# Optimization experiments

Hardware: AMD Instinct MI355X
Metric: run time of the kernel (lower is better)

## Reference

```python
import jax, jax.numpy as jnp
import numpy as np

C, NSET, K, GC = 64, 32, 3, 4
G = C // GC          # 16 KBA groups
EPS = 1e-6


def conv2d(x, w, b=None, groups=1, padding=0):
    out = jax.lax.conv_general_dilated(
        x, w, (1, 1), [(padding, padding), (padding, padding)],
        dimension_numbers=('NCHW', 'OIHW', 'NCHW'), feature_group_count=groups)
    if b is not None:
        out = out + b[None, :, None, None]
    return out


def layernorm2d(x, w, b):
    mu = jnp.mean(x, axis=1, keepdims=True)
    var = jnp.var(x, axis=1, keepdims=True)
    return (x - mu) / jnp.sqrt(var + EPS) * w[None, :, None, None] + b[None, :, None, None]


def simple_gate(x):
    a, b = jnp.split(x, 2, axis=1)
    return a * b


def kba(x, att, kb_b, kb_w):
    # x: [B,C,H,W], att: [B,nset,H,W], kb_b: [1,nset,C], kb_w: [1,nset,C*(C//G)*K*K]
    B, C_, H, W = x.shape
    KK = K * K
    cg = C_ // G  # channels per group
    att2 = att.reshape(B, NSET, H * W).transpose(0, 2, 1)            # [B,HW,nset]
    bias = att2 @ kb_b[0]                                             # [B,HW,C]
    attk = (att2 @ kb_w[0]).reshape(B, H * W, G, cg, cg * KK)         # per-pixel kernels
    pad = K // 2
    xp = jnp.pad(x, ((0, 0), (0, 0), (pad, pad), (pad, pad)))
    # torch.unfold ordering: feature index = c*KK + ki*K + kj
    patches = jnp.stack([xp[:, :, i:i + H, j:j + W]
                         for i in range(K) for j in range(K)], axis=2)  # [B,C,KK,H,W]
    uf = patches.reshape(B, G, cg * KK, H * W).transpose(0, 3, 1, 2)    # [B,HW,G,cg*KK]
    out = jnp.einsum('bpgod,bpgd->bpgo', attk, uf).reshape(B, H * W, C_) + bias
    return out.transpose(0, 2, 1).reshape(B, C_, H, W)


def fca(x, fc1_w, fc1_b, fc2_w, fc2_b, fsca_w, fsca_b):
    f = jnp.fft.fft2(x, norm='ortho')                      # over (H,W)
    cf = jnp.concatenate([f.real, f.imag], axis=1)         # [B,2C,H,W]
    t = conv2d(simple_gate(conv2d(cf, fc1_w, fc1_b)), fc2_w, fc2_b)
    r, im = jnp.split(t, 2, axis=1)
    ra = conv2d(jnp.mean(r, axis=(2, 3), keepdims=True), fsca_w, fsca_b)
    ia = conv2d(jnp.mean(im, axis=(2, 3), keepdims=True), fsca_w, fsca_b)
    fn = (r + r * ra) + 1j * (im + im * ia)
    return jnp.abs(jnp.fft.ifft2(fn, norm='ortho'))


def reference(inp, n1_w, n1_b, n2_w, n2_b, sca_w, sca_b, c11a_w, c11a_b, c11b_w, c11b_b,
              c1_w, c1_b, c21_w, c21_b, c2a_w, c2a_b, c2c_w, c2c_b, c211_w, c211_b,
              c3_w, c3_b, kb_w, kb_b, ga1, attgamma, beta, gamma,
              fc1_w, fc1_b, fc2_w, fc2_b, fsca_w, fsca_b):
    x = layernorm2d(inp, n1_w, n1_b)
    sca = conv2d(jnp.mean(x, axis=(2, 3), keepdims=True), sca_w, sca_b)
    x1 = conv2d(conv2d(x, c11a_w, c11a_b), c11b_w, c11b_b, groups=C // 4, padding=2)
    att = conv2d(simple_gate(conv2d(x, c2a_w, c2a_b, groups=32, padding=1)),
                 c2c_w, c2c_b) * attgamma + conv2d(x, c211_w, c211_b)
    uf = conv2d(conv2d(x, c1_w, c1_b), c21_w, c21_b, groups=C, padding=1)
    xk = kba(uf, att, kb_b, kb_w) * ga1 + uf
    x = xk * x1 * sca
    x = conv2d(x, c3_w, c3_b)
    y = inp + x * beta
    z = fca(layernorm2d(y, n2_w, n2_b), fc1_w, fc1_b, fc2_w, fc2_b, fsca_w, fsca_b)
    return y + z * gamma


def setup_inputs() -> dict:
    key = jax.random.key(0)
    B, H, W = 2, 160, 160
    ks = jax.random.split(key, 32)
    def rn(i, shape, s=0.05):
        return jax.random.normal(ks[i], shape, dtype=jnp.float32) * s
    return dict(
        inp=rn(0, (B, C, H, W), 1.0),
        n1_w=jnp.ones((C,), jnp.float32), n1_b=jnp.zeros((C,), jnp.float32),
        n2_w=jnp.ones((C,), jnp.float32), n2_b=jnp.zeros((C,), jnp.float32),
        sca_w=rn(1, (C, C, 1, 1)), sca_b=rn(2, (C,)),
        c11a_w=rn(3, (C, C, 1, 1)), c11a_b=rn(4, (C,)),
        c11b_w=rn(5, (C, 4, 5, 5)), c11b_b=rn(6, (C,)),
        c1_w=rn(7, (C, C, 1, 1)), c1_b=rn(8, (C,)),
        c21_w=rn(9, (C, 1, 3, 3)), c21_b=rn(10, (C,)),
        c2a_w=rn(11, (32, 2, 3, 3)), c2a_b=rn(12, (32,)),
        c2c_w=rn(13, (NSET, 16, 1, 1)), c2c_b=rn(14, (NSET,)),
        c211_w=rn(15, (NSET, C, 1, 1)), c211_b=rn(16, (NSET,)),
        c3_w=rn(17, (C, C, 1, 1)), c3_b=rn(18, (C,)),
        kb_w=rn(19, (1, NSET, C * (C // G) * K * K)),
        kb_b=rn(20, (1, NSET, C)),
        ga1=jnp.full((1, C, 1, 1), 0.01, jnp.float32),
        attgamma=jnp.full((1, NSET, 1, 1), 0.01, jnp.float32),
        beta=jnp.full((1, C, 1, 1), 0.01, jnp.float32),
        gamma=jnp.full((1, C, 1, 1), 0.01, jnp.float32),
        fc1_w=rn(21, (4 * C, 2 * C, 1, 1)), fc1_b=rn(22, (4 * C,)),
        fc2_w=rn(23, (2 * C, 2 * C, 1, 1)), fc2_b=rn(24, (2 * C,)),
        fsca_w=rn(25, (C, C, 1, 1)), fsca_b=rn(26, (C,)),
    )
```

## Files before the change

### kernel.cpp

```cpp
#include <hip/hip_runtime.h>
#include <hip/hip_bf16.h>

typedef __hip_bfloat16 bf16;
typedef __attribute__((ext_vector_type(8))) short short8;
typedef __attribute__((ext_vector_type(4))) float f32x4;
typedef __attribute__((ext_vector_type(4))) unsigned short u16x4;

#define Hh 160
#define Wd 160
#define HWp (Hh*Wd)
#define Bn 2
#define Cc 64
#define NPIX (Bn*HWp)
#define SCL 0.07905694150420949f
#define TWO_PI_160 0.039269908169872414f

static __device__ __forceinline__ float b2f(bf16 x) { return __bfloat162float(x); }
static __device__ __forceinline__ bf16 f2b(float f) { return __float2bfloat16(f); }
static __device__ __forceinline__ unsigned short f2bu(float f) {
  union { bf16 h; unsigned short u; } z; z.h = __float2bfloat16(f); return z.u;
}
static __device__ __forceinline__ float ubf(unsigned short u) {
  union { unsigned int i; float f; } z; z.i = ((unsigned int)u) << 16; return z.f;
}

__global__ void k_ln(const float* __restrict__ in, const float* __restrict__ w,
                     const float* __restrict__ bb, bf16* __restrict__ out) {
  __shared__ float2 sm[4][64];
  int t = threadIdx.x;
  int pxl = t & 63, cq = t >> 6;
  int pix = blockIdx.x * 64 + pxl;
  int b = pix / HWp, p = pix - b * HWp;
  const float* src = in + ((size_t)b * Cc + cq * 16) * HWp + p;
  float v[16];
  float s = 0.f, s2 = 0.f;
  #pragma unroll
  for (int i = 0; i < 16; i++) {
    v[i] = src[(size_t)i * HWp];
    s += v[i]; s2 += v[i] * v[i];
  }
  sm[cq][pxl] = make_float2(s, s2);
  __syncthreads();
  float S = 0.f, S2 = 0.f;
  #pragma unroll
  for (int k = 0; k < 4; k++) { float2 z = sm[k][pxl]; S += z.x; S2 += z.y; }
  float mu = S * (1.f / 64.f);
  float var = S2 * (1.f / 64.f) - mu * mu;
  float rs = rsqrtf(fmaxf(var, 0.f) + 1e-6f);
  bf16* dst = out + ((size_t)b * Cc + cq * 16) * HWp + p;
  #pragma unroll
  for (int i = 0; i < 16; i++) {
    int c = cq * 16 + i;
    dst[(size_t)i * HWp] = f2b((v[i] - mu) * rs * w[c] + bb[c]);
  }
}

__global__ void k_meanhw(const bf16* __restrict__ in, float* __restrict__ out) {
  int bc = blockIdx.x;
  const bf16* src = in + (size_t)bc * HWp;
  int t = threadIdx.x;
  float s = 0.f;
  for (int i = t; i < HWp; i += 256) s += b2f(src[i]);
  __shared__ float sm[256];
  sm[t] = s; __syncthreads();
  for (int off = 128; off; off >>= 1) { if (t < off) sm[t] += sm[t + off]; __syncthreads(); }
  if (t == 0) out[bc] = sm[0] * (1.f / HWp);
}

__global__ void k_meanhw2(const bf16* __restrict__ in0, const bf16* __restrict__ in1,
                          float* __restrict__ out) {
  int bc = blockIdx.x;
  const bf16* src = (bc < 128) ? (in0 + (size_t)bc * HWp) : (in1 + (size_t)(bc - 128) * HWp);
  int t = threadIdx.x;
  float s = 0.f;
  for (int i = t; i < HWp; i += 256) s += b2f(src[i]);
  __shared__ float sm[256];
  sm[t] = s; __syncthreads();
  for (int off = 128; off; off >>= 1) { if (t < off) sm[t] += sm[t + off]; __syncthreads(); }
  if (t == 0) out[bc] = sm[0] * (1.f / HWp);
}

__global__ void k_small_mv(const float* __restrict__ xin, const float* __restrict__ w,
                           const float* __restrict__ bias, float* __restrict__ out, int addone) {
  int t = threadIdx.x;
  int b = t >> 6, o = t & 63;
  float acc = bias[o];
  for (int k = 0; k < 64; k++) acc += w[o * 64 + k] * xin[b * 64 + k];
  out[t] = addone ? (1.f + acc) : acc;
}

__global__ void k_small_mv2(const float* __restrict__ xin, const float* __restrict__ w,
                            const float* __restrict__ bias, float* __restrict__ out) {
  int t = threadIdx.x;
  int half = t >> 7, r = t & 127;
  int b = r >> 6, o = r & 63;
  const float* x = xin + half * 128 + b * 64;
  float acc = bias[o];
  for (int k = 0; k < 64; k++) acc += w[o * 64 + k] * x[k];
  out[half * 128 + r] = 1.f + acc;
}

__global__ void k_c2a4(const bf16* __restrict__ in, const float* __restrict__ w,
                       const float* __restrict__ bias, bf16* __restrict__ out) {
  int t = threadIdx.x;
  int o = blockIdx.y, b = blockIdx.z;
  int pq = blockIdx.x * 256 + t;
  int h = pq / 40, x4 = (pq - h * 40) * 4;
  float bs = bias[o];
  float acc[4] = {bs, bs, bs, bs};
  #pragma unroll
  for (int ci = 0; ci < 2; ci++) {
    const unsigned short* src = (const unsigned short*)in + ((size_t)b * Cc + o * 2 + ci) * HWp;
    float wv[9];
    #pragma unroll
    for (int i = 0; i < 9; i++) wv[i] = w[(o * 2 + ci) * 9 + i];
    #pragma unroll
    for (int ki = 0; ki < 3; ki++) {
      int hh = h + ki - 1;
      if ((unsigned)hh >= Hh) continue;
      const unsigned short* row = src + hh * Wd + x4;
      float v[6];
      u16x4 m = *(const u16x4*)row;
      v[1] = ubf(m[0]); v[2] = ubf(m[1]); v[3] = ubf(m[2]); v[4] = ubf(m[3]);
      v[0] = (x4 > 0) ? ubf(row[-1]) : 0.f;
      v[5] = (x4 + 4 < Wd) ? ubf(row[4]) : 0.f;
      #pragma unroll
      for (int j = 0; j < 4; j++)
        #pragma unroll
        for (int kj = 0; kj < 3; kj++)
          acc[j] = fmaf(wv[ki * 3 + kj], v[j + kj], acc[j]);
    }
  }
  u16x4 pk;
  #pragma unroll
  for (int j = 0; j < 4; j++) pk[j] = f2bu(acc[j]);
  *(u16x4*)((unsigned short*)out + ((size_t)b * 32 + o) * HWp + h * Wd + x4) = pk;
}

__global__ void k_c21dw4(const bf16* __restrict__ in, const float* __restrict__ w,
                         const float* __restrict__ bias, bf16* __restrict__ out) {
  int t = threadIdx.x;
  int c = blockIdx.y, b = blockIdx.z;
  int pq = blockIdx.x * 256 + t;
  int h = pq / 40, x4 = (pq - h * 40) * 4;
  const unsigned short* src = (const unsigned short*)in + ((size_t)b * Cc + c) * HWp;
  float wv[9];
  #pragma unroll
  for (int i = 0; i < 9; i++) wv[i] = w[c * 9 + i];
  float bs = bias[c];
  float acc[4] = {bs, bs, bs, bs};
  #pragma unroll
  for (int ki = 0; ki < 3; ki++) {
    int hh = h + ki - 1;
    if ((unsigned)hh >= Hh) continue;
    const unsigned short* row = src + hh * Wd + x4;
    float v[6];
    u16x4 m = *(const u16x4*)row;
    v[1] = ubf(m[0]); v[2] = ubf(m[1]); v[3] = ubf(m[2]); v[4] = ubf(m[3]);
    v[0] = (x4 > 0) ? ubf(row[-1]) : 0.f;
    v[5] = (x4 + 4 < Wd) ? ubf(row[4]) : 0.f;
    #pragma unroll
    for (int j = 0; j < 4; j++)
      #pragma unroll
      for (int kj = 0; kj < 3; kj++)
        acc[j] = fmaf(wv[ki * 3 + kj], v[j + kj], acc[j]);
  }
  u16x4 pk;
  #pragma unroll
  for (int j = 0; j < 4; j++) pk[j] = f2bu(acc[j]);
  *(u16x4*)((unsigned short*)out + ((size_t)b * Cc + c) * HWp + h * Wd + x4) = pk;
}

__global__ void k_prep_all(const float* __restrict__ kbw, const float* __restrict__ kbb,
                           short* __restrict__ kbwF,
                           const float* __restrict__ fc1w, const float* __restrict__ fc2w,
                           short* __restrict__ wAf1, short* __restrict__ wAf2,
                           short* __restrict__ cosF, short* __restrict__ sinF,
                           const float* __restrict__ c11aw, const float* __restrict__ c1w,
                           const float* __restrict__ c3w, const float* __restrict__ c2cw,
                           const float* __restrict__ c211w, const float* __restrict__ attg,
                           short* __restrict__ wA_c11a, short* __restrict__ wA_c1,
                           short* __restrict__ wA_c3, short* __restrict__ wA_att) {
  int i = blockIdx.x * 256 + threadIdx.x;
  if (i < 81920) {
    int g = i / 5120, r = i - g * 5120;
    float v = 0.f;
    if (r < 4096) {
      int j = r & 7, lane = (r >> 3) & 63, mt = r >> 9;
      int m = mt * 16 + (lane & 15);
      int s = m >> 2, o = m & 3;
      int k = (lane >> 4) * 8 + j;
      v = kbw[s * 2304 + g * 144 + o * 36 + k];
    } else {
      int r2 = r - 4096;
      int j = r2 & 7, n = (r2 >> 3) & 15, mt = r2 >> 7;
      int m = mt * 16 + n;
      int s = m >> 2, o = m & 3;
      int k = 32 + j;
      if (k < 36) v = kbw[s * 2304 + g * 144 + o * 36 + k];
      else if (k == 36) v = kbb[s * 64 + g * 4 + o];
    }
    kbwF[i] = (short)f2bu(v);
  } else if (i < 131072) {
    int i1 = i - 81920;
    if (i1 < 32768) {
      int j = i1 & 7, lane = (i1 >> 3) & 63, fk = i1 >> 9;
      int kc = fk & 3, mt = fk >> 2;
      int o = mt * 16 + (lane & 15);
      int k = kc * 32 + (lane >> 4) * 8 + j;
      wAf1[i1] = (short)f2bu(fc1w[o * 128 + k]);
    } else {
      int i2 = i1 - 32768;
      int j = i2 & 7, lane = (i2 >> 3) & 63, fk = i2 >> 9;
      int kc = fk & 3, mt = fk >> 2;
      int o = mt * 16 + (lane & 15);
      int k = kc * 32 + (lane >> 4) * 8 + j;
      wAf2[i2] = (short)f2bu(fc2w[o * 128 + k]);
    }
  } else if (i < 156672) {
    int i2 = i - 131072;
    int j = i2 & 7, lane = (i2 >> 3) & 63, fk = i2 >> 9;
    int kc = fk % 5, ct = fk / 5;
    int c = ct * 16 + (lane & 15);
    int bb2 = kc * 32 + (lane >> 4) * 8 + j;
    int m = (bb2 * c) % 160;
    float sv, cv;
    __sincosf((float)m * TWO_PI_160, &sv, &cv);
    cosF[i2] = (short)f2bu(cv);
    sinF[i2] = (short)f2bu(sv);
  } else {
    int i3 = i - 156672;
    if (i3 < 12288) {
      int wi = i3 / 4096, r = i3 - wi * 4096;
      int j = r & 7, lane = (r >> 3) & 63, fk = r >> 9;
      int kc = fk & 1, mt = fk >> 1;
      int o = mt * 16 + (lane & 15);
      int k = kc * 32 + (lane >> 4) * 8 + j;
      const float* w = (wi == 0) ? c11aw : (wi == 1) ? c1w : c3w;
      short* dst = (wi == 0) ? wA_c11a : (wi == 1) ? wA_c1 : wA_c3;
      dst[r] = (short)f2bu(w[o * 64 + k]);
    } else {
      int r = i3 - 12288;
      int j = r & 7, lane = (r >> 3) & 63, fk = r >> 9;
      int kc = fk % 3, mt = fk / 3;
      int s = mt * 16 + (lane & 15);
      int k = kc * 32 + (lane >> 4) * 8 + j;
      float v;
      if (k < 16) v = c2cw[s * 16 + k] * attg[s];
      else if (k < 32) v = 0.f;
      else v = c211w[s * 64 + (k - 32)];
      wA_att[r] = (short)f2bu(v);
    }
  }
}

__global__ __launch_bounds__(256) void k_conv1x1_mfma(
    const bf16* __restrict__ in, const short* __restrict__ wA,
    const float* __restrict__ bias, bf16* __restrict__ out) {
  int b = blockIdx.z;
  int lane = threadIdx.x & 63, w = threadIdx.x >> 6;
  int px = blockIdx.x * 64 + w * 16 + (lane & 15);
  int q = lane >> 4;
  const unsigned short* src = (const unsigned short*)in + (size_t)b * Cc * HWp;
  const short8* wf = (const short8*)wA;
  f32x4 acc[4];
  #pragma unroll
  for (int mt = 0; mt < 4; mt++) acc[mt] = (f32x4){0.f, 0.f, 0.f, 0.f};
  #pragma unroll
  for (int kc = 0; kc < 2; kc++) {
    short8 bfv;
    #pragma unroll
    for (int j = 0; j < 8; j++) bfv[j] = (short)src[(size_t)(kc * 32 + q * 8 + j) * HWp + px];
    #pragma unroll
    for (int mt = 0; mt < 4; mt++) {
      short8 af = wf[(mt * 2 + kc) * 64 + lane];
      acc[mt] = __builtin_amdgcn_mfma_f32_16x16x32_bf16(af, bfv, acc[mt], 0, 0, 0);
    }
  }
  unsigned short* dst = (unsigned short*)out + (size_t)b * Cc * HWp;
  #pragma unroll
  for (int mt = 0; mt < 4; mt++)
    #pragma unroll
    for (int j = 0; j < 4; j++) {
      int o = mt * 16 + q * 4 + j;
      dst[(size_t)o * HWp + px] = f2bu(acc[mt][j] + bias[o]);
    }
}

__global__ __launch_bounds__(256) void k_c3y_ln2(
    const bf16* __restrict__ in, const short* __restrict__ wA,
    const float* __restrict__ bias, const float* __restrict__ beta,
    const float* __restrict__ inp, float* __restrict__ y,
    const float* __restrict__ n2w, const float* __restrict__ n2b,
    bf16* __restrict__ Xout) {
  int b = blockIdx.z;
  int lane = threadIdx.x & 63, w = threadIdx.x >> 6;
  int px = blockIdx.x * 64 + w * 16 + (lane & 15);
  int q = lane >> 4;
  const unsigned short* src = (const unsigned short*)in + (size_t)b * Cc * HWp;
  const short8* wf = (const short8*)wA;
  f32x4 acc[4];
  #pragma unroll
  for (int mt = 0; mt < 4; mt++) acc[mt] = (f32x4){0.f, 0.f, 0.f, 0.f};
  #pragma unroll
  for (int kc = 0; kc < 2; kc++) {
    short8 bfv;
    #pragma unroll
    for (int j = 0; j < 8; j++) bfv[j] = (short)src[(size_t)(kc * 32 + q * 8 + j) * HWp + px];
    #pragma unroll
    for (int mt = 0; mt < 4; mt++) {
      short8 af = wf[(mt * 2 + kc) * 64 + lane];
      acc[mt] = __builtin_amdgcn_mfma_f32_16x16x32_bf16(af, bfv, acc[mt], 0, 0, 0);
    }
  }
  float yv[4][4];
  float s = 0.f, s2 = 0.f;
  #pragma unroll
  for (int mt = 0; mt < 4; mt++)
    #pragma unroll
    for (int j = 0; j < 4; j++) {
      int o = mt * 16 + q * 4 + j;
      size_t oi = ((size_t)b * Cc + o) * HWp + px;
      float v = inp[oi] + (acc[mt][j] + bias[o]) * beta[o];
      y[oi] = v;
      yv[mt][j] = v;
      s += v; s2 += v * v;
    }
  s  += __shfl_xor(s, 16);  s  += __shfl_xor(s, 32);
  s2 += __shfl_xor(s2, 16); s2 += __shfl_xor(s2, 32);
  float mu = s * (1.f / 64.f);
  float var = s2 * (1.f / 64.f) - mu * mu;
  float rs = rsqrtf(fmaxf(var, 0.f) + 1e-6f);
  unsigned short* Xu = (unsigned short*)Xout + (size_t)b * Cc * HWp;
  #pragma unroll
  for (int mt = 0; mt < 4; mt++)
    #pragma unroll
    for (int j = 0; j < 4; j++) {
      int o = mt * 16 + q * 4 + j;
      Xu[(size_t)o * HWp + px] = f2bu((yv[mt][j] - mu) * rs * n2w[o] + n2b[o]);
    }
}

__global__ __launch_bounds__(256) void k_att_mfma(
    const bf16* __restrict__ g, const bf16* __restrict__ x,
    const short* __restrict__ wA, const float* __restrict__ c2cb,
    const float* __restrict__ c211b, const float* __restrict__ attg,
    bf16* __restrict__ att) {
  int b = blockIdx.z;
  int lane = threadIdx.x & 63, w = threadIdx.x >> 6;
  int px = blockIdx.x * 64 + w * 16 + (lane & 15);
  int q = lane >> 4;
  const unsigned short* gs = (const unsigned short*)g + (size_t)b * 32 * HWp;
  const unsigned short* xs = (const unsigned short*)x + (size_t)b * Cc * HWp;
  const short8* wf = (const short8*)wA;
  f32x4 acc[2];
  acc[0] = (f32x4){0.f, 0.f, 0.f, 0.f};
  acc[1] = (f32x4){0.f, 0.f, 0.f, 0.f};
  {
    short8 bfv;
    #pragma unroll
    for (int j = 0; j < 8; j++) {
      int k = q * 8 + j;
      short v = 0;
      if (q < 2) {
        float gv = ubf(gs[(size_t)k * HWp + px]) * ubf(gs[(size_t)(16 + k) * HWp + px]);
        v = (short)f2bu(gv);
      }
      bfv[j] = v;
    }
    #pragma unroll
    for (int mt = 0; mt < 2; mt++) {
      short8 af = wf[(mt * 3 + 0) * 64 + lane];
      acc[mt] = __builtin_amdgcn_mfma_f32_16x16x32_bf16(af, bfv, acc[mt], 0, 0, 0);
    }
  }
  #pragma unroll
  for (int kc = 1; kc < 3; kc++) {
    short8 bfv;
    #pragma unroll
    for (int j = 0; j < 8; j++)
      bfv[j] = (short)xs[(size_t)((kc - 1) * 32 + q * 8 + j) * HWp + px];
    #pragma unroll
    for (int mt = 0; mt < 2; mt++) {
      short8 af = wf[(mt * 3 + kc) * 64 + lane];
      acc[mt] = __builtin_amdgcn_mfma_f32_16x16x32_bf16(af, bfv, acc[mt], 0, 0, 0);
    }
  }
  unsigned short* dst = (unsigned short*)att + (size_t)b * 32 * HWp;
  #pragma unroll
  for (int mt = 0; mt < 2; mt++)
    #pragma unroll
    for (int j = 0; j < 4; j++) {
      int s = mt * 16 + q * 4 + j;
      dst[(size_t)s * HWp + px] = f2bu(acc[mt][j] + c2cb[s] * attg[s] + c211b[s]);
    }
}

__global__ __launch_bounds__(256) void k_c11b_direct(
    const bf16* __restrict__ t1, const float* __restrict__ w,
    const float* __restrict__ bias, bf16* __restrict__ out) {
  __shared__ float xs[4 * 20 * 68];
  __shared__ float wsm[4 * 5 * 4 * 5];
  __shared__ float bsm[4];
  int bz = blockIdx.z;
  int b = bz >> 4, g = bz & 15;
  int h0 = blockIdx.y * 16;
  int w0 = blockIdx.x * 64;
  int t = threadIdx.x;
  for (int i = t; i < 400; i += 256) {
    int kj = i % 5, rem = i / 5;
    int o = rem & 3; rem >>= 2;
    int ki = rem % 5, ci = rem / 5;
    wsm[i] = w[((g * 4 + o) * 4 + ci) * 25 + ki * 5 + kj];
  }
  if (t < 4) bsm[t] = bias[g * 4 + t];
  const unsigned short* src = (const unsigned short*)t1 + ((size_t)b * Cc + g * 4) * HWp;
  for (int i = t; i < 4 * 20 * 68; i += 256) {
    int ci = i / 1360, rem2 = i - ci * 1360;
    int r = rem2 / 68, col = rem2 - r * 68;
    int hh = h0 + r - 2, ww = w0 + col - 2;
    float v = 0.f;
    if ((unsigned)hh < Hh && (unsigned)ww < Wd)
      v = ubf(src[(size_t)ci * HWp + hh * Wd + ww]);
    xs[i] = v;
  }
  __syncthreads();
  int wq = t & 15, hq = t >> 4;
  float acc[4][4];
  #pragma unroll
  for (int o = 0; o < 4; o++)
    #pragma unroll
    for (int j = 0; j < 4; j++) acc[o][j] = bsm[o];
  #pragma unroll
  for (int ci = 0; ci < 4; ci++) {
    #pragma unroll
    for (int ki = 0; ki < 5; ki++) {
      const float* wrow = &wsm[(ci * 5 + ki) * 20];
      float wv[20];
      #pragma unroll
      for (int x = 0; x < 20; x++) wv[x] = wrow[x];
      const float* xrow = &xs[ci * 1360 + (hq + ki) * 68 + wq * 4];
      float xv[8];
      #pragma unroll
      for (int x = 0; x < 8; x++) xv[x] = xrow[x];
      #pragma unroll
      for (int o = 0; o < 4; o++)
        #pragma unroll
        for (int j = 0; j < 4; j++)
          #pragma unroll
          for (int kj = 0; kj < 5; kj++)
            acc[o][j] = fmaf(wv[o * 5 + kj], xv[j + kj], acc[o][j]);
    }
  }
  int width = Wd - w0;
  if (wq * 4 < width) {
    unsigned short* dst = (unsigned short*)out + ((size_t)b * Cc + g * 4) * HWp
                        + (h0 + hq) * Wd + w0 + wq * 4;
    #pragma unroll
    for (int o = 0; o < 4; o++) {
      u16x4 pk;
      #pragma unroll
      for (int j = 0; j < 4; j++) pk[j] = f2bu(acc[o][j]);
      *(u16x4*)(dst + (size_t)o * HWp) = pk;
    }
  }
}

__global__ __launch_bounds__(256) void k_kba_mfma(
    const bf16* __restrict__ uf, const bf16* __restrict__ att,
    const bf16* __restrict__ x1, const float* __restrict__ scaV,
    const short* __restrict__ kbwF, const float* __restrict__ ga1,
    bf16* __restrict__ out) {
  __shared__ short8 fragL[1280];
  __shared__ unsigned short patchL[8 * 3 * 66];
  __shared__ unsigned short attL[64][33];
  int bz = blockIdx.z;
  int b = bz >> 3, gp = bz & 7;
  int h = blockIdx.y;
  int w0 = blockIdx.x * 64;
  int width = min(64, Wd - w0);
  int t = threadIdx.x;
  int c0 = gp * 8;
  const short8* src8 = (const short8*)kbwF + (size_t)gp * 1280;
  #pragma unroll
  for (int i = 0; i < 5; i++) fragL[t + i * 256] = src8[t + i * 256];
  const unsigned short* uf_u = (const unsigned short*)uf;
  for (int i = t; i < 8 * 3 * 66; i += 256) {
    int cl = i / 198, rem = i - cl * 198;
    int r = rem / 66, col = rem - r * 66;
    int hh = h + r - 1, ww = w0 + col - 1;
    unsigned short v = 0;
    if ((unsigned)hh < Hh && (unsigned)ww < Wd)
      v = uf_u[((size_t)b * Cc + c0 + cl) * HWp + hh * Wd + ww];
    patchL[i] = v;
  }
  const unsigned short* att_u = (const unsigned short*)att + (size_t)b * 32 * HWp;
  for (int i = t; i < 64 * 32; i += 256) {
    int px = i & 63, s = i >> 6;
    unsigned short v = 0;
    if (px < width) v = att_u[(size_t)s * HWp + h * Wd + w0 + px];
    attL[px][s] = v;
  }
  __syncthreads();
  int lane = t & 63, w = t >> 6;
  int n = lane & 15, q = lane >> 4;
  int pxl = w * 16 + n;
  float attR[8];
  #pragma unroll
  for (int mt = 0; mt < 8; mt++) attR[mt] = ubf(attL[pxl][4 * mt + q]);
  int offA[8];
  #pragma unroll
  for (int j = 0; j < 8; j++) {
    int k = q * 8 + j;
    int ci = k / 9, r = k - ci * 9, ki = r / 3, kj = r - ki * 3;
    offA[j] = ci * 198 + ki * 66 + pxl + kj;
  }
  int offB[4];
  #pragma unroll
  for (int j = 0; j < 4; j++) {
    int k = 32 + j, r = k - 27, ki = r / 3, kj = r - ki * 3;
    offB[j] = 3 * 198 + ki * 66 + pxl + kj;
  }
  const unsigned short* x1u = (const unsigned short*)x1 + (size_t)b * Cc * HWp + h * Wd + w0;
  unsigned short* outu = (unsigned short*)out + (size_t)b * Cc * HWp + h * Wd + w0;
  #pragma unroll
  for (int gl = 0; gl < 2; gl++) {
    int g = gp * 2 + gl;
    const short8* fgl = fragL + gl * 640;
    short8 b0, b1;
    #pragma unroll
    for (int j = 0; j < 8; j++) b0[j] = (short)patchL[gl * 792 + offA[j]];
    #pragma unroll
    for (int j = 0; j < 8; j++) b1[j] = 0;
    if (q == 0) {
      #pragma unroll
      for (int j = 0; j < 4; j++) b1[j] = (short)patchL[gl * 792 + offB[j]];
      b1[4] = (short)0x3F80;
    }
    f32x4 acc[8];
    #pragma unroll
    for (int mt = 0; mt < 8; mt++) acc[mt] = (f32x4){0.f, 0.f, 0.f, 0.f};
    #pragma unroll
    for (int mt = 0; mt < 8; mt++) {
      short8 a0 = fgl[mt * 64 + lane];
      acc[mt] = __builtin_amdgcn_mfma_f32_16x16x32_bf16(a0, b0, acc[mt], 0, 0, 0);
      short8 a1 = (short8){0,0,0,0,0,0,0,0};
      if (q == 0) a1 = fgl[512 + mt * 16 + n];
      acc[mt] = __builtin_amdgcn_mfma_f32_16x16x32_bf16(a1, b1, acc[mt], 0, 0, 0);
    }
    #pragma unroll
    for (int o = 0; o < 4; o++) {
      float P = 0.f;
      #pragma unroll
      for (int mt = 0; mt < 8; mt++) P += attR[mt] * acc[mt][o];
      P += __shfl_xor(P, 16);
      P += __shfl_xor(P, 32);
      if (o == q && pxl < width) {
        int c = g * 4 + q;
        float ufc = ubf(patchL[(gl * 4 + q) * 198 + 66 + pxl + 1]);
        float xk = P * ga1[c] + ufc;
        float xv = xk * ubf(x1u[(size_t)c * HWp + pxl]) * scaV[b * 64 + c];
        outu[(size_t)c * HWp + pxl] = f2bu(xv);
      }
    }
  }
}

__global__ __launch_bounds__(64) void k_cpass_mfma(
    const bf16* __restrict__ inr, const bf16* __restrict__ ini,
    const short* __restrict__ cosF, const short* __restrict__ sinF,
    bf16* __restrict__ outr, bf16* __restrict__ outi,
    float sgn, float scale,
    const float* __restrict__ sclr, const float* __restrict__ scli) {
  int plane = blockIdx.z;
  int a0 = blockIdx.x * 16;
  int cth = blockIdx.y * 5;
  int lane = threadIdx.x;
  int n = lane & 15, q = lane >> 4;
  const unsigned short* pr = (const unsigned short*)inr + (size_t)plane * HWp;
  const unsigned short* pi = ini ? (const unsigned short*)ini + (size_t)plane * HWp : nullptr;
  float srm = sclr ? sclr[plane] : 1.f;
  float sim = scli ? scli[plane] : 1.f;
  short8 br[5], bi[5];
  #pragma unroll
  for (int kc = 0; kc < 5; kc++) {
    br[kc] = *(const short8*)(pr + (a0 + n) * 160 + kc * 32 + q * 8);
    if (pi) bi[kc] = *(const short8*)(pi + (a0 + n) * 160 + kc * 32 + q * 8);
  }
  const short8* cf = (const short8*)cosF;
  const short8* sf = (const short8*)sinF;
  unsigned short* qr = (unsigned short*)outr + (size_t)plane * HWp;
  unsigned short* qi = (unsigned short*)outi + (size_t)plane * HWp;
  for (int ctl = 0; ctl < 5; ctl++) {
    int ct = cth + ctl;
    f32x4 arr = (f32x4){0.f,0.f,0.f,0.f}, asr = (f32x4){0.f,0.f,0.f,0.f};
    f32x4 ari = (f32x4){0.f,0.f,0.f,0.f}, asi = (f32x4){0.f,0.f,0.f,0.f};
    #pragma unroll
    for (int kc = 0; kc < 5; kc++) {
      short8 ca = cf[(ct * 5 + kc) * 64 + lane];
      short8 sa = sf[(ct * 5 + kc) * 64 + lane];
      arr = __builtin_amdgcn_mfma_f32_16x16x32_bf16(ca, br[kc], arr, 0, 0, 0);
      asr = __builtin_amdgcn_mfma_f32_16x16x32_bf16(sa, br[kc], asr, 0, 0, 0);
      if (pi) {
        ari = __builtin_amdgcn_mfma_f32_16x16x32_bf16(ca, bi[kc], ari, 0, 0, 0);
        asi = __builtin_amdgcn_mfma_f32_16x16x32_bf16(sa, bi[kc], asi, 0, 0, 0);
      }
    }
    #pragma unroll
    for (int j = 0; j < 4; j++) {
      int c = ct * 16 + q * 4 + j;
      float xc = srm * arr[j], xs = srm * asr[j];
      float ic = pi ? sim * ari[j] : 0.f, is = pi ? sim * asi[j] : 0.f;
      float orv = (xc - sgn * is) * scale;
      float oiv = (sgn * xs + ic) * scale;
      qr[c * 160 + a0 + n] = f2bu(orv);
      qi[c * 160 + a0 + n] = f2bu(oiv);
    }
  }
}

__global__ __launch_bounds__(64) void k_cpass_final_mfma(
    const bf16* __restrict__ inr, const bf16* __restrict__ ini,
    const short* __restrict__ cosF, const short* __restrict__ sinF,
    float sgn, float scale,
    const float* __restrict__ gamma, float* __restrict__ dout) {
  int plane = blockIdx.z;
  int a0 = blockIdx.x * 16;
  int cth = blockIdx.y * 5;
  int lane = threadIdx.x;
  int n = lane & 15, q = lane >> 4;
  const unsigned short* pr = (const unsigned short*)inr + (size_t)plane * HWp;
  const unsigned short* pi = (const unsigned short*)ini + (size_t)plane * HWp;
  short8 br[5], bi[5];
  #pragma unroll
  for (int kc = 0; kc < 5; kc++) {
    br[kc] = *(const short8*)(pr + (a0 + n) * 160 + kc * 32 + q * 8);
    bi[kc] = *(const short8*)(pi + (a0 + n) * 160 + kc * 32 + q * 8);
  }
  const short8* cf = (const short8*)cosF;
  const short8* sf = (const short8*)sinF;
  float gm = gamma[plane & 63];
  float* dp = dout + (size_t)plane * HWp;
  for (int ctl = 0; ctl < 5; ctl++) {
    int ct = cth + ctl;
    f32x4 arr = (f32x4){0.f,0.f,0.f,0.f}, asr = (f32x4){0.f,0.f,0.f,0.f};
    f32x4 ari = (f32x4){0.f,0.f,0.f,0.f}, asi = (f32x4){0.f,0.f,0.f,0.f};
    #pragma unroll
    for (int kc = 0; kc < 5; kc++) {
      short8 ca = cf[(ct * 5 + kc) * 64 + lane];
      short8 sa = sf[(ct * 5 + kc) * 64 + lane];
      arr = __builtin_amdgcn_mfma_f32_16x16x32_bf16(ca, br[kc], arr, 0, 0, 0);
      asr = __builtin_amdgcn_mfma_f32_16x16x32_bf16(sa, br[kc], asr, 0, 0, 0);
      ari = __builtin_amdgcn_mfma_f32_16x16x32_bf16(ca, bi[kc], ari, 0, 0, 0);
      asi = __builtin_amdgcn_mfma_f32_16x16x32_bf16(sa, bi[kc], asi, 0, 0, 0);
    }
    #pragma unroll
    for (int j = 0; j < 4; j++) {
      int c = ct * 16 + q * 4 + j;
      float orv = (arr[j] - sgn * asi[j]) * scale;
      float oiv = (sgn * asr[j] + ari[j]) * scale;
      float z = sqrtf(orv * orv + oiv * oiv);
      dp[c * 160 + a0 + n] += z * gm;
    }
  }
}

__global__ __launch_bounds__(256) void k_fc1_mfma(
    const bf16* __restrict__ Fr, const bf16* __restrict__ Fi,
    const short* __restrict__ wA, const float* __restrict__ bias,
    bf16* __restrict__ G1, bf16* __restrict__ G2) {
  int b = blockIdx.z;
  int lane = threadIdx.x & 63, w = threadIdx.x >> 6;
  int px = blockIdx.x * 64 + w * 16 + (lane & 15);
  int q = lane >> 4;
  const unsigned short* fr = (const unsigned short*)Fr + (size_t)b * Cc * HWp;
  const unsigned short* fi = (const unsigned short*)Fi + (size_t)b * Cc * HWp;
  const short8* wf = (const short8*)wA;
  f32x4 acc[16];
  #pragma unroll
  for (int mt = 0; mt < 16; mt++) acc[mt] = (f32x4){0.f, 0.f, 0.f, 0.f};
  #pragma unroll
  for (int kc = 0; kc < 4; kc++) {
    const unsigned short* basep = (kc < 2) ? (fr + (size_t)(kc * 32) * HWp)
                                           : (fi + (size_t)((kc - 2) * 32) * HWp);
    short8 bfv;
    #pragma unroll
    for (int j = 0; j < 8; j++) bfv[j] = (short)basep[(size_t)(q * 8 + j) * HWp + px];
    #pragma unroll
    for (int mt = 0; mt < 16; mt++) {
      short8 af = wf[(mt * 4 + kc) * 64 + lane];
      acc[mt] = __builtin_amdgcn_mfma_f32_16x16x32_bf16(af, bfv, acc[mt], 0, 0, 0);
    }
  }
  unsigned short* g1 = (unsigned short*)G1 + (size_t)b * Cc * HWp;
  unsigned short* g2 = (unsigned short*)G2 + (size_t)b * Cc * HWp;
  #pragma unroll
  for (int mt = 0; mt < 8; mt++)
    #pragma unroll
    for (int j = 0; j < 4; j++) {
      int o = mt * 16 + q * 4 + j;
      float v1 = acc[mt][j] + bias[o];
      float v2 = acc[mt + 8][j] + bias[o + 128];
      unsigned short hv = f2bu(v1 * v2);
      if (o < 64) g1[(size_t)o * HWp + px] = hv;
      else        g2[(size_t)(o - 64) * HWp + px] = hv;
    }
}

__global__ __launch_bounds__(256) void k_fc2_mfma(
    const bf16* __restrict__ G1, const bf16* __restrict__ G2,
    const short* __restrict__ wA, const float* __restrict__ bias,
    bf16* __restrict__ Or, bf16* __restrict__ Oi) {
  int b = blockIdx.z;
  int lane = threadIdx.x & 63, w = threadIdx.x >> 6;
  int px = blockIdx.x * 64 + w * 16 + (lane & 15);
  int q = lane >> 4;
  const unsigned short* g1 = (const unsigned short*)G1 + (size_t)b * Cc * HWp;
  const unsigned short* g2 = (const unsigned short*)G2 + (size_t)b * Cc * HWp;
  const short8* wf = (const short8*)wA;
  f32x4 acc[8];
  #pragma unroll
  for (int mt = 0; mt < 8; mt++) acc[mt] = (f32x4){0.f, 0.f, 0.f, 0.f};
  #pragma unroll
  for (int kc = 0; kc < 4; kc++) {
    const unsigned short* basep = (kc < 2) ? (g1 + (size_t)(kc * 32) * HWp)
                                           : (g2 + (size_t)((kc - 2) * 32) * HWp);
    short8 bfv;
    #pragma unroll
    for (int j = 0; j < 8; j++) bfv[j] = (short)basep[(size_t)(q * 8 + j) * HWp + px];
    #pragma unroll
    for (int mt = 0; mt < 8; mt++) {
      short8 af = wf[(mt * 4 + kc) * 64 + lane];
      acc[mt] = __builtin_amdgcn_mfma_f32_16x16x32_bf16(af, bfv, acc[mt], 0, 0, 0);
    }
  }
  unsigned short* orp = (unsigned short*)Or + (size_t)b * Cc * HWp;
  unsigned short* oip = (unsigned short*)Oi + (size_t)b * Cc * HWp;
  #pragma unroll
  for (int mt = 0; mt < 8; mt++)
    #pragma unroll
    for (int j = 0; j < 4; j++) {
      int o = mt * 16 + q * 4 + j;
      unsigned short hv = f2bu(acc[mt][j] + bias[o]);
      if (o < 64) orp[(size_t)o * HWp + px] = hv;
      else        oip[(size_t)(o - 64) * HWp + px] = hv;
    }
}

extern "C" void kernel_launch(void* const* d_in, const int* in_sizes, int n_in,
                              void* d_out, int out_size, void* d_ws, size_t ws_size,
                              hipStream_t stream) {
  const float* inp   = (const float*)d_in[0];
  const float* n1w   = (const float*)d_in[1];
  const float* n1b   = (const float*)d_in[2];
  const float* n2w   = (const float*)d_in[3];
  const float* n2b   = (const float*)d_in[4];
  const float* scaw  = (const float*)d_in[5];
  const float* scab  = (const float*)d_in[6];
  const float* c11aw = (const float*)d_in[7];
  const float* c11ab = (const float*)d_in[8];
  const float* c11bw = (const float*)d_in[9];
  const float* c11bb = (const float*)d_in[10];
  const float* c1w   = (const float*)d_in[11];
  const float* c1b   = (const float*)d_in[12];
  const float* c21w  = (const float*)d_in[13];
  const float* c21b  = (const float*)d_in[14];
  const float* c2aw  = (const float*)d_in[15];
  const float* c2ab  = (const float*)d_in[16];
  const float* c2cw  = (const float*)d_in[17];
  const float* c2cb  = (const float*)d_in[18];
  const float* c211w = (const float*)d_in[19];
  const float* c211b = (const float*)d_in[20];
  const float* c3w   = (const float*)d_in[21];
  const float* c3b   = (const float*)d_in[22];
  const float* kbw   = (const float*)d_in[23];
  const float* kbb   = (const float*)d_in[24];
  const float* ga1   = (const float*)d_in[25];
  const float* attg  = (const float*)d_in[26];
  const float* beta  = (const float*)d_in[27];
  const float* gamma = (const float*)d_in[28];
  const float* fc1w  = (const float*)d_in[29];
  const float* fc1b  = (const float*)d_in[30];
  const float* fc2w  = (const float*)d_in[31];
  const float* fc2b  = (const float*)d_in[32];
  const float* fscaw = (const float*)d_in[33];
  const float* fscab = (const float*)d_in[34];

  const size_t S = (size_t)Bn * Cc * HWp;
  bf16* A  = (bf16*)d_ws;
  bf16* Bs = A + S;
  bf16* Cs = A + 2 * S;
  bf16* Ds = A + 3 * S;
  float* smalls = (float*)(A + 4 * S);
  float* xm   = smalls;
  float* scaV = smalls + 128;
  float* rmv  = smalls + 256;
  float* sra  = smalls + 512;
  short* wS   = (short*)(smalls + 1024);
  short* wAf1 = wS;
  short* wAf2 = wAf1 + 32768;
  short* cosF = wAf2 + 16384;
  short* sinF = cosF + 25600;
  short* wA_c11a = sinF + 25600;
  short* wA_c1   = wA_c11a + 4096;
  short* wA_c3   = wA_c1 + 4096;
  short* wA_att  = wA_c3 + 4096;
  short* kbwF    = wA_att + 3072;
  bf16* gbuf = Bs;
  bf16* attb = Bs + S / 2;
  float* yb  = (float*)d_out;

  dim3 cgrid(10, 2, Bn * Cc);
  dim3 pgrid(400, 1, Bn);

  k_prep_all<<<dim3(672), dim3(256), 0, stream>>>(kbw, kbb, kbwF, fc1w, fc2w, wAf1, wAf2,
                                                  cosF, sinF, c11aw, c1w, c3w, c2cw, c211w,
                                                  attg, wA_c11a, wA_c1, wA_c3, wA_att);
  k_ln<<<dim3(800), dim3(256), 0, stream>>>(inp, n1w, n1b, A);
  k_meanhw<<<dim3(128), dim3(256), 0, stream>>>(A, xm);
  k_small_mv<<<dim3(1), dim3(128), 0, stream>>>(xm, scaw, scab, scaV, 0);
  k_conv1x1_mfma<<<pgrid, dim3(256), 0, stream>>>(A, wA_c11a, c11ab, Bs);
  k_c11b_direct<<<dim3(3, 10, Bn * 16), dim3(256), 0, stream>>>(Bs, c11bw, c11bb, Cs);
  k_c2a4<<<dim3(25, 32, Bn), dim3(256), 0, stream>>>(A, c2aw, c2ab, gbuf);
  k_att_mfma<<<pgrid, dim3(256), 0, stream>>>(gbuf, A, wA_att, c2cb, c211b, attg, attb);
  k_conv1x1_mfma<<<pgrid, dim3(256), 0, stream>>>(A, wA_c1, c1b, Ds);
  k_c21dw4<<<dim3(25, 64, Bn), dim3(256), 0, stream>>>(Ds, c21w, c21b, A);
  k_kba_mfma<<<dim3(3, 160, Bn * 8), dim3(256), 0, stream>>>(A, attb, Cs, scaV, kbwF, ga1, Ds);
  k_c3y_ln2<<<pgrid, dim3(256), 0, stream>>>(Ds, wA_c3, c3b, beta, inp, yb, n2w, n2b, A);
  k_cpass_mfma<<<cgrid, dim3(64), 0, stream>>>(A, (const bf16*)nullptr, cosF, sinF, Bs, Cs, -1.f, SCL, nullptr, nullptr);
  k_cpass_mfma<<<cgrid, dim3(64), 0, stream>>>(Bs, Cs, cosF, sinF, Ds, A, -1.f, SCL, nullptr, nullptr);
  k_fc1_mfma<<<pgrid, dim3(256), 0, stream>>>(Ds, A, wAf1, fc1b, Bs, Cs);
  k_fc2_mfma<<<pgrid, dim3(256), 0, stream>>>(Bs, Cs, wAf2, fc2b, Ds, A);
  k_meanhw2<<<dim3(256), dim3(256), 0, stream>>>(Ds, A, rmv);
  k_small_mv2<<<dim3(1), dim3(256), 0, stream>>>(rmv, fscaw, fscab, sra);
  k_cpass_mfma<<<cgrid, dim3(64), 0, stream>>>(Ds, A, cosF, sinF, Bs, Cs, 1.f, SCL, sra, sra + 128);
  k_cpass_final_mfma<<<cgrid, dim3(64), 0, stream>>>(Bs, Cs, cosF, sinF, 1.f, SCL, gamma, yb);
}
```

Measured before the change: 445.9 us.

## Fuse c11a/c1 1x1 convs and fold depthwise conv into KBA kernel

The two 1x1 MFMA convolutions that read the same input are merged into one dual-output kernel, so the input is loaded once. The depthwise 3x3 conv (c21) is no longer a separate kernel. It is computed inside the KBA kernel from a 5-row halo tile loaded into shared memory, which removes a full intermediate write and read. Buffer assignments for the downstream FFT and FC passes are rotated to match. The trade-off is extra shared memory, an extra barrier, and recomputing the depthwise conv on halo pixels in each KBA block.

```diff
diff --git a/kernel.cpp b/kernel.cpp
--- a/kernel.cpp
+++ b/kernel.cpp
@@ -135,40 +135,6 @@
   #pragma unroll
   for (int j = 0; j < 4; j++) pk[j] = f2bu(acc[j]);
   *(u16x4*)((unsigned short*)out + ((size_t)b * 32 + o) * HWp + h * Wd + x4) = pk;
-}
-
-__global__ void k_c21dw4(const bf16* __restrict__ in, const float* __restrict__ w,
-                         const float* __restrict__ bias, bf16* __restrict__ out) {
-  int t = threadIdx.x;
-  int c = blockIdx.y, b = blockIdx.z;
-  int pq = blockIdx.x * 256 + t;
-  int h = pq / 40, x4 = (pq - h * 40) * 4;
-  const unsigned short* src = (const unsigned short*)in + ((size_t)b * Cc + c) * HWp;
-  float wv[9];
-  #pragma unroll
-  for (int i = 0; i < 9; i++) wv[i] = w[c * 9 + i];
-  float bs = bias[c];
-  float acc[4] = {bs, bs, bs, bs};
-  #pragma unroll
-  for (int ki = 0; ki < 3; ki++) {
-    int hh = h + ki - 1;
-    if ((unsigned)hh >= Hh) continue;
-    const unsigned short* row = src + hh * Wd + x4;
-    float v[6];
-    u16x4 m = *(const u16x4*)row;
-    v[1] = ubf(m[0]); v[2] = ubf(m[1]); v[3] = ubf(m[2]); v[4] = ubf(m[3]);
-    v[0] = (x4 > 0) ? ubf(row[-1]) : 0.f;
-    v[5] = (x4 + 4 < Wd) ? ubf(row[4]) : 0.f;
-    #pragma unroll
-    for (int j = 0; j < 4; j++)
-      #pragma unroll
-      for (int kj = 0; kj < 3; kj++)
-        acc[j] = fmaf(wv[ki * 3 + kj], v[j + kj], acc[j]);
-  }
-  u16x4 pk;
-  #pragma unroll
-  for (int j = 0; j < 4; j++) pk[j] = f2bu(acc[j]);
-  *(u16x4*)((unsigned short*)out + ((size_t)b * Cc + c) * HWp + h * Wd + x4) = pk;
 }
 
 __global__ void k_prep_all(const float* __restrict__ kbw, const float* __restrict__ kbb,
@@ -254,18 +220,23 @@
   }
 }
 
-__global__ __launch_bounds__(256) void k_conv1x1_mfma(
-    const bf16* __restrict__ in, const short* __restrict__ wA,
-    const float* __restrict__ bias, bf16* __restrict__ out) {
+__global__ __launch_bounds__(256) void k_conv1x1_dual(
+    const bf16* __restrict__ in, const short* __restrict__ wA1,
+    const float* __restrict__ b1, const short* __restrict__ wA2,
+    const float* __restrict__ b2, bf16* __restrict__ out1, bf16* __restrict__ out2) {
   int b = blockIdx.z;
   int lane = threadIdx.x & 63, w = threadIdx.x >> 6;
   int px = blockIdx.x * 64 + w * 16 + (lane & 15);
   int q = lane >> 4;
   const unsigned short* src = (const unsigned short*)in + (size_t)b * Cc * HWp;
-  const short8* wf = (const short8*)wA;
-  f32x4 acc[4];
-  #pragma unroll
-  for (int mt = 0; mt < 4; mt++) acc[mt] = (f32x4){0.f, 0.f, 0.f, 0.f};
+  const short8* wf1 = (const short8*)wA1;
+  const short8* wf2 = (const short8*)wA2;
+  f32x4 acc1[4], acc2[4];
+  #pragma unroll
+  for (int mt = 0; mt < 4; mt++) {
+    acc1[mt] = (f32x4){0.f, 0.f, 0.f, 0.f};
+    acc2[mt] = (f32x4){0.f, 0.f, 0.f, 0.f};
+  }
   #pragma unroll
   for (int kc = 0; kc < 2; kc++) {
     short8 bfv;
@@ -273,17 +244,21 @@
     for (int j = 0; j < 8; j++) bfv[j] = (short)src[(size_t)(kc * 32 + q * 8 + j) * HWp + px];
     #pragma unroll
     for (int mt = 0; mt < 4; mt++) {
-      short8 af = wf[(mt * 2 + kc) * 64 + lane];
-      acc[mt] = __builtin_amdgcn_mfma_f32_16x16x32_bf16(af, bfv, acc[mt], 0, 0, 0);
-    }
-  }
-  unsigned short* dst = (unsigned short*)out + (size_t)b * Cc * HWp;
+      short8 a1 = wf1[(mt * 2 + kc) * 64 + lane];
+      acc1[mt] = __builtin_amdgcn_mfma_f32_16x16x32_bf16(a1, bfv, acc1[mt], 0, 0, 0);
+      short8 a2 = wf2[(mt * 2 + kc) * 64 + lane];
+      acc2[mt] = __builtin_amdgcn_mfma_f32_16x16x32_bf16(a2, bfv, acc2[mt], 0, 0, 0);
+    }
+  }
+  unsigned short* d1 = (unsigned short*)out1 + (size_t)b * Cc * HWp;
+  unsigned short* d2 = (unsigned short*)out2 + (size_t)b * Cc * HWp;
   #pragma unroll
   for (int mt = 0; mt < 4; mt++)
     #pragma unroll
     for (int j = 0; j < 4; j++) {
       int o = mt * 16 + q * 4 + j;
-      dst[(size_t)o * HWp + px] = f2bu(acc[mt][j] + bias[o]);
+      d1[(size_t)o * HWp + px] = f2bu(acc1[mt][j] + b1[o]);
+      d2[(size_t)o * HWp + px] = f2bu(acc2[mt][j] + b2[o]);
     }
 }
 
@@ -467,13 +442,16 @@
 }
 
 __global__ __launch_bounds__(256) void k_kba_mfma(
-    const bf16* __restrict__ uf, const bf16* __restrict__ att,
+    const bf16* __restrict__ t2, const bf16* __restrict__ att,
     const bf16* __restrict__ x1, const float* __restrict__ scaV,
     const short* __restrict__ kbwF, const float* __restrict__ ga1,
+    const float* __restrict__ c21w, const float* __restrict__ c21b,
     bf16* __restrict__ out) {
   __shared__ short8 fragL[1280];
+  __shared__ unsigned short t2L[8 * 5 * 68];
   __shared__ unsigned short patchL[8 * 3 * 66];
   __shared__ unsigned short attL[64][33];
+  __shared__ float wdw[80];
   int bz = blockIdx.z;
   int b = bz >> 3, gp = bz & 7;
   int h = blockIdx.y;
@@ -484,22 +462,42 @@
   const short8* src8 = (const short8*)kbwF + (size_t)gp * 1280;
   #pragma unroll
   for (int i = 0; i < 5; i++) fragL[t + i * 256] = src8[t + i * 256];
-  const unsigned short* uf_u = (const unsigned short*)uf;
-  for (int i = t; i < 8 * 3 * 66; i += 256) {
-    int cl = i / 198, rem = i - cl * 198;
-    int r = rem / 66, col = rem - r * 66;
-    int hh = h + r - 1, ww = w0 + col - 1;
+  const unsigned short* t2u = (const unsigned short*)t2;
+  for (int i = t; i < 8 * 5 * 68; i += 256) {
+    int cl = i / 340, rem = i - cl * 340;
+    int r = rem / 68, col = rem - r * 68;
+    int hh = h + r - 2, ww = w0 + col - 2;
     unsigned short v = 0;
     if ((unsigned)hh < Hh && (unsigned)ww < Wd)
-      v = uf_u[((size_t)b * Cc + c0 + cl) * HWp + hh * Wd + ww];
-    patchL[i] = v;
-  }
+      v = t2u[((size_t)b * Cc + c0 + cl) * HWp + hh * Wd + ww];
+    t2L[i] = v;
+  }
+  if (t < 72) wdw[t] = c21w[(c0 + t / 9) * 9 + t % 9];
+  else if (t < 80) wdw[t] = c21b[c0 + (t - 72)];
   const unsigned short* att_u = (const unsigned short*)att + (size_t)b * 32 * HWp;
   for (int i = t; i < 64 * 32; i += 256) {
     int px = i & 63, s = i >> 6;
     unsigned short v = 0;
     if (px < width) v = att_u[(size_t)s * HWp + h * Wd + w0 + px];
     attL[px][s] = v;
+  }
+  __syncthreads();
+  for (int i = t; i < 8 * 3 * 66; i += 256) {
+    int cl = i / 198, rem = i - cl * 198;
+    int r = rem / 66, col = rem - r * 66;
+    int hh = h + r - 1, ww = w0 + col - 1;
+    unsigned short v = 0;
+    if ((unsigned)hh < Hh && (unsigned)ww < Wd) {
+      float acc = wdw[72 + cl];
+      const float* wc = &wdw[cl * 9];
+      #pragma unroll
+      for (int ki = 0; ki < 3; ki++)
+        #pragma unroll
+        for (int kj = 0; kj < 3; kj++)
+          acc = fmaf(wc[ki * 3 + kj], ubf(t2L[cl * 340 + (r + ki) * 68 + col + kj]), acc);
+      v = f2bu(acc);
+    }
+    patchL[i] = v;
   }
   __syncthreads();
   int lane = t & 63, w = t >> 6;
@@ -819,20 +817,19 @@
   k_ln<<<dim3(800), dim3(256), 0, stream>>>(inp, n1w, n1b, A);
   k_meanhw<<<dim3(128), dim3(256), 0, stream>>>(A, xm);
   k_small_mv<<<dim3(1), dim3(128), 0, stream>>>(xm, scaw, scab, scaV, 0);
-  k_conv1x1_mfma<<<pgrid, dim3(256), 0, stream>>>(A, wA_c11a, c11ab, Bs);
+  k_conv1x1_dual<<<pgrid, dim3(256), 0, stream>>>(A, wA_c11a, c11ab, wA_c1, c1b, Bs, Ds);
   k_c11b_direct<<<dim3(3, 10, Bn * 16), dim3(256), 0, stream>>>(Bs, c11bw, c11bb, Cs);
   k_c2a4<<<dim3(25, 32, Bn), dim3(256), 0, stream>>>(A, c2aw, c2ab, gbuf);
   k_att_mfma<<<pgrid, dim3(256), 0, stream>>>(gbuf, A, wA_att, c2cb, c211b, attg, attb);
-  k_conv1x1_mfma<<<pgrid, dim3(256), 0, stream>>>(A, wA_c1, c1b, Ds);
-  k_c21dw4<<<dim3(25, 64, Bn), dim3(256), 0, stream>>>(Ds, c21w, c21b, A);
-  k_kba_mfma<<<dim3(3, 160, Bn * 8), dim3(256), 0, stream>>>(A, attb, Cs, scaV, kbwF, ga1, Ds);
-  k_c3y_ln2<<<pgrid, dim3(256), 0, stream>>>(Ds, wA_c3, c3b, beta, inp, yb, n2w, n2b, A);
-  k_cpass_mfma<<<cgrid, dim3(64), 0, stream>>>(A, (const bf16*)nullptr, cosF, sinF, Bs, Cs, -1.f, SCL, nullptr, nullptr);
-  k_cpass_mfma<<<cgrid, dim3(64), 0, stream>>>(Bs, Cs, cosF, sinF, Ds, A, -1.f, SCL, nullptr, nullptr);
-  k_fc1_mfma<<<pgrid, dim3(256), 0, stream>>>(Ds, A, wAf1, fc1b, Bs, Cs);
-  k_fc2_mfma<<<pgrid, dim3(256), 0, stream>>>(Bs, Cs, wAf2, fc2b, Ds, A);
-  k_meanhw2<<<dim3(256), dim3(256), 0, stream>>>(Ds, A, rmv);
+  k_kba_mfma<<<dim3(3, 160, Bn * 8), dim3(256), 0, stream>>>(Ds, attb, Cs, scaV, kbwF, ga1,
+                                                             c21w, c21b, A);
+  k_c3y_ln2<<<pgrid, dim3(256), 0, stream>>>(A, wA_c3, c3b, beta, inp, yb, n2w, n2b, Bs);
+  k_cpass_mfma<<<cgrid, dim3(64), 0, stream>>>(Bs, (const bf16*)nullptr, cosF, sinF, Cs, Ds, -1.f, SCL, nullptr, nullptr);
+  k_cpass_mfma<<<cgrid, dim3(64), 0, stream>>>(Cs, Ds, cosF, sinF, A, Bs, -1.f, SCL, nullptr, nullptr);
+  k_fc1_mfma<<<pgrid, dim3(256), 0, stream>>>(A, Bs, wAf1, fc1b, Cs, Ds);
+  k_fc2_mfma<<<pgrid, dim3(256), 0, stream>>>(Cs, Ds, wAf2, fc2b, A, Bs);
+  k_meanhw2<<<dim3(256), dim3(256), 0, stream>>>(A, Bs, rmv);
   k_small_mv2<<<dim3(1), dim3(256), 0, stream>>>(rmv, fscaw, fscab, sra);
-  k_cpass_mfma<<<cgrid, dim3(64), 0, stream>>>(Ds, A, cosF, sinF, Bs, Cs, 1.f, SCL, sra, sra + 128);
-  k_cpass_final_mfma<<<cgrid, dim3(64), 0, stream>>>(Bs, Cs, cosF, sinF, 1.f, SCL, gamma, yb);
-}
+  k_cpass_mfma<<<cgrid, dim3(64), 0, stream>>>(A, Bs, cosF, sinF, Cs, Ds, 1.f, SCL, sra, sra + 128);
+  k_cpass_final_mfma<<<cgrid, dim3(64), 0, stream>>>(Cs, Ds, cosF, sinF, 1.f, SCL, gamma, yb);
+}
```

Result: slower. 466.3 us (+4.6%).
